# Kernel optimization log

Measured on AMD Instinct MI355X. Metric: run time of the kernel, lower is better.

The kernel has to match this reference:

```python
import jax, jax.numpy as jnp
import numpy as np

B, N, H, O = 2, 512, 128, 32  # batch, n_particles, hidden_dim, obs_dim


def _linear_init(key, out_d, in_d):
    kw, kb = jax.random.split(key)
    s = 1.0 / np.sqrt(in_d)
    W = jax.random.uniform(kw, (out_d, in_d), minval=-s, maxval=s, dtype=jnp.float32)
    b = jax.random.uniform(kb, (out_d,), minval=-s, maxval=s, dtype=jnp.float32)
    return W, b


def setup_inputs() -> dict:
    key = jax.random.key(0)
    ks = jax.random.split(key, 8)
    z = jax.random.normal(ks[0], (B, N, H), dtype=jnp.float32)
    s_t = jax.random.normal(ks[1], (B, N, O), dtype=jnp.float32)
    W1, b1 = _linear_init(ks[2], H, 2 * H)   # relation_mlp layer 0
    W2, b2 = _linear_init(ks[3], H, H)       # relation_mlp layer 2
    Wq, bq = _linear_init(ks[4], H, H)       # query_proj
    Wk, bk = _linear_init(ks[5], H, O)       # key_proj
    W3, b3 = _linear_init(ks[6], H, H)       # aggregation_mlp layer 0
    W4, b4 = _linear_init(ks[7], H, H)       # aggregation_mlp layer 2
    return dict(z=z, s_t=s_t, W1=W1, b1=b1, W2=W2, b2=b2, Wq=Wq, bq=bq,
                Wk=Wk, bk=bk, W3=W3, b3=b3, W4=W4, b4=b4)


def reference(z, s_t, W1, b1, W2, b2, Wq, bq, Wk, bk, W3, b3, W4, b4):
    b_, n, h = z.shape
    # query depends only on i, key only on j (repeat in the original is redundant)
    q = z @ Wq.T + bq            # [B,N,H]
    k = s_t @ Wk.T + bk          # [B,N,H]
    scores = jnp.einsum('bih,bjh->bij', q, k) / (h ** 0.5)   # [B,N,N]
    eye = jnp.eye(n, dtype=bool)
    scores = jnp.where(eye, -jnp.inf, scores)
    attn = jax.nn.softmax(scores, axis=-1)                   # [B,N,N]
    # relation_mlp on concat(z_i, z_j): split first weight into i- and j- halves
    W1i, W1j = W1[:, :h], W1[:, h:]
    zi = z @ W1i.T               # [B,N,H]
    zj = z @ W1j.T               # [B,N,H]
    rel = jnp.tanh(zi[:, :, None, :] + zj[:, None, :, :] + b1) @ W2.T + b2  # [B,N,N,H]
    agg = jnp.einsum('bij,bijh->bih', attn, rel)             # weighted sum over j
    dz_dt = jnp.tanh(agg @ W3.T + b3) @ W4.T + b4
    return dz_dt
```

## Files before the change

kernel.cpp:

```cpp
#include <hip/hip_runtime.h>
#include <hip/hip_bf16.h>

#define NN 512
#define HH 128
#define OO 32

#define KL 2.8853900817779268f

__device__ __forceinline__ float vexp2(float x) {
    float r; asm("v_exp_f32 %0, %1" : "=v"(r) : "v"(x)); return r;
}
__device__ __forceinline__ float vrcp(float x) {
    float r; asm("v_rcp_f32 %0, %1" : "=v"(r) : "v"(x)); return r;
}
__device__ __forceinline__ float tanh_fast(float x) {
    float e = vexp2(KL * x);
    return 1.0f - 2.0f * vrcp(e + 1.0f);
}
__device__ __forceinline__ float waveRedMax(float v) {
#pragma unroll
    for (int off = 32; off > 0; off >>= 1) v = fmaxf(v, __shfl_xor(v, off, 64));
    return v;
}
__device__ __forceinline__ float waveRedSum(float v) {
#pragma unroll
    for (int off = 32; off > 0; off >>= 1) v += __shfl_xor(v, off, 64);
    return v;
}
__device__ __forceinline__ float red8(float v) {
    v += __shfl_xor(v, 1, 64); v += __shfl_xor(v, 2, 64); v += __shfl_xor(v, 4, 64);
    return v;
}
__device__ __forceinline__ float dot16r(const float4* w, const float* x, int rot) {
    float a = 0;
#pragma unroll
    for (int ii = 0; ii < 4; ii++) {
        int i = (ii + rot) & 3;
        float4 xv = *(const float4*)(x + i * 4);
        a = fmaf(xv.x, w[ii].x, a); a = fmaf(xv.y, w[ii].y, a);
        a = fmaf(xv.z, w[ii].z, a); a = fmaf(xv.w, w[ii].w, a);
    }
    return a;
}
__device__ __forceinline__ unsigned short f2bf(float x) {
    unsigned u = __float_as_uint(x);
    u += 0x7fffu + ((u >> 16) & 1u);
    return (unsigned short)(u >> 16);
}
__device__ __forceinline__ float bf_lo(unsigned u) { return __uint_as_float((u & 0xffffu) << 16); }
__device__ __forceinline__ float bf_hi(unsigned u) { return __uint_as_float(u & 0xffff0000u); }

__global__ __launch_bounds__(1024, 4) void prep_kernel(
    const float* __restrict__ z, const float* __restrict__ s_t,
    const float* __restrict__ W1, const float* __restrict__ b1,
    const float* __restrict__ Wq, const float* __restrict__ bq,
    const float* __restrict__ Wk, const float* __restrict__ bk,
    float* __restrict__ qP, float* __restrict__ cP,
    unsigned short* __restrict__ EzjG, float* __restrict__ kTG) {
    __shared__ float zrow[4][HH];
    __shared__ float srow[4][OO];
    int t = threadIdx.x, bid = blockIdx.x;
    int r0 = bid * 4, b = bid >> 7, i0 = (bid & 127) * 4;
    int kq = t & 7, h = t >> 3, rot = (kq >> 1) & 3;

    const float4* WqP = (const float4*)(Wq + (size_t)h * HH) + kq * 4;
    const float4* WiP = (const float4*)(W1 + (size_t)h * 2 * HH) + kq * 4;
    const float4* WjP = (const float4*)(W1 + (size_t)h * 2 * HH + HH) + kq * 4;
    float4 wq[4], wi[4], wj[4];
#pragma unroll
    for (int ii = 0; ii < 4; ii++) {
        wq[ii] = WqP[(ii + rot) & 3];
        wi[ii] = WiP[(ii + rot) & 3];
        wj[ii] = WjP[(ii + rot) & 3];
    }
    float4 wk = ((const float4*)(Wk + (size_t)h * OO))[kq];
    float vbq = bq[h], vb1 = b1[h], vbk = bk[h];

    if (t < 4 * HH) zrow[t >> 7][t & 127] = z[(size_t)r0 * HH + t];
    else if (t < 4 * HH + 4 * OO) {
        int u = t - 4 * HH;
        srow[u >> 5][u & 31] = s_t[(size_t)r0 * OO + u];
    }
    __syncthreads();

    {
        float a0 = red8(dot16r(wq, &zrow[0][kq * 16], rot));
        float a1 = red8(dot16r(wq, &zrow[1][kq * 16], rot));
        float a2 = red8(dot16r(wq, &zrow[2][kq * 16], rot));
        float a3 = red8(dot16r(wq, &zrow[3][kq * 16], rot));
        if (kq == 0) {
            float* qp = qP + (size_t)bid * 512 + h * 4;
            qp[0] = a0 + vbq; qp[1] = a1 + vbq; qp[2] = a2 + vbq; qp[3] = a3 + vbq;
        }
    }
    {
        float a0 = red8(dot16r(wi, &zrow[0][kq * 16], rot));
        float a1 = red8(dot16r(wi, &zrow[1][kq * 16], rot));
        float a2 = red8(dot16r(wi, &zrow[2][kq * 16], rot));
        float a3 = red8(dot16r(wi, &zrow[3][kq * 16], rot));
        if (kq == 0) {
            float* cp = cP + (size_t)bid * 512 + h * 4;
            cp[0] = vexp2(KL * (a0 + vb1)); cp[1] = vexp2(KL * (a1 + vb1));
            cp[2] = vexp2(KL * (a2 + vb1)); cp[3] = vexp2(KL * (a3 + vb1));
        }
    }
    {
        float a0 = red8(dot16r(wj, &zrow[0][kq * 16], rot));
        float a1 = red8(dot16r(wj, &zrow[1][kq * 16], rot));
        float a2 = red8(dot16r(wj, &zrow[2][kq * 16], rot));
        float a3 = red8(dot16r(wj, &zrow[3][kq * 16], rot));
        if (kq == 0) {
            EzjG[(size_t)(r0 + 0) * HH + h] = f2bf(vexp2(KL * a0));
            EzjG[(size_t)(r0 + 1) * HH + h] = f2bf(vexp2(KL * a1));
            EzjG[(size_t)(r0 + 2) * HH + h] = f2bf(vexp2(KL * a2));
            EzjG[(size_t)(r0 + 3) * HH + h] = f2bf(vexp2(KL * a3));
        }
    }
    {
        float4 s0 = *(const float4*)&srow[0][kq * 4];
        float4 s1 = *(const float4*)&srow[1][kq * 4];
        float4 s2 = *(const float4*)&srow[2][kq * 4];
        float4 s3 = *(const float4*)&srow[3][kq * 4];
        float a0 = red8(s0.x * wk.x + s0.y * wk.y + s0.z * wk.z + s0.w * wk.w);
        float a1 = red8(s1.x * wk.x + s1.y * wk.y + s1.z * wk.z + s1.w * wk.w);
        float a2 = red8(s2.x * wk.x + s2.y * wk.y + s2.z * wk.z + s2.w * wk.w);
        float a3 = red8(s3.x * wk.x + s3.y * wk.y + s3.z * wk.z + s3.w * wk.w);
        if (kq == 0) {
            float4 kv = make_float4(a0 + vbk, a1 + vbk, a2 + vbk, a3 + vbk);
            *(float4*)(kTG + ((size_t)b * HH + h) * NN + i0) = kv;
        }
    }
}

__global__ __launch_bounds__(1024, 4) void fused_kernel(
    const float* __restrict__ qP, const float* __restrict__ cP,
    const float* __restrict__ kTG, const unsigned short* __restrict__ EzjG,
    const float* __restrict__ W2, const float* __restrict__ b2,
    const float* __restrict__ W3, const float* __restrict__ b3,
    const float* __restrict__ W4, const float* __restrict__ b4,
    float* __restrict__ out) {
    __shared__ float q4T[HH][4];
    __shared__ float c4T[HH][4];
    __shared__ float attnT[NN][4];
    __shared__ float buf[8192];
    __shared__ float UL[4][HH];
    __shared__ float aggL[4][HH];
    __shared__ float h1L[4][HH];
    __shared__ float redA[16], redB[16], redC[16], redD[16];

    float (*scp)[4][NN] = (float (*)[4][NN])buf;
    float (*part)[4][HH] = (float (*)[4][HH])buf;

    int t = threadIdx.x, bid = blockIdx.x;
    int b = bid >> 7, i0 = (bid & 127) * 4, r0 = bid * 4;

    if (t < 512) ((float*)q4T)[t] = qP[(size_t)bid * 512 + t];
    else         ((float*)c4T)[t - 512] = cP[(size_t)bid * 512 + (t - 512)];

    int j = t & 511, hs = t >> 9, h0 = hs * 64;
    const float* kb = kTG + ((size_t)b * HH + h0) * NN + j;
    float kv[32];
#pragma unroll
    for (int hh = 0; hh < 32; hh++) kv[hh] = kb[(size_t)hh * NN];
    __syncthreads();

    float s0 = 0, s1 = 0, s2 = 0, s3 = 0;
#pragma unroll
    for (int hh = 0; hh < 32; hh++) {
        float4 qv = *(const float4*)q4T[h0 + hh];
        s0 = fmaf(qv.x, kv[hh], s0); s1 = fmaf(qv.y, kv[hh], s1);
        s2 = fmaf(qv.z, kv[hh], s2); s3 = fmaf(qv.w, kv[hh], s3);
    }
#pragma unroll
    for (int hh = 0; hh < 32; hh++) kv[hh] = kb[(size_t)(32 + hh) * NN];
#pragma unroll
    for (int hh = 0; hh < 32; hh++) {
        float4 qv = *(const float4*)q4T[h0 + 32 + hh];
        s0 = fmaf(qv.x, kv[hh], s0); s1 = fmaf(qv.y, kv[hh], s1);
        s2 = fmaf(qv.z, kv[hh], s2); s3 = fmaf(qv.w, kv[hh], s3);
    }
    scp[hs][0][j] = s0; scp[hs][1][j] = s1;
    scp[hs][2][j] = s2; scp[hs][3][j] = s3;

    int lane6 = t & 63, qs = t >> 6, hp = lane6 * 2, jb = qs * 32;
    const unsigned* zbU = (const unsigned*)EzjG + (size_t)b * NN * (HH / 2) + lane6;
    unsigned uv[32];
#pragma unroll
    for (int jj = 0; jj < 32; jj++) uv[jj] = zbU[(size_t)(jb + jj) * (HH / 2)];
    __syncthreads();

    {
        int rp = t >> 9;
        int lr0 = rp * 2, lr1 = lr0 + 1;
        const float sc = 0.08838834764831845f;
        float c0 = (scp[0][lr0][j] + scp[1][lr0][j]) * sc;
        float c1 = (scp[0][lr1][j] + scp[1][lr1][j]) * sc;
        if (j == i0 + lr0) c0 = -1e30f;
        if (j == i0 + lr1) c1 = -1e30f;
        int lane = t & 63, w = t >> 6, wb = rp * 8;
        float m0 = waveRedMax(c0), m1 = waveRedMax(c1);
        if (lane == 0) { redA[w] = m0; redB[w] = m1; }
        __syncthreads();
        float mm0 = redA[wb], mm1 = redB[wb];
#pragma unroll
        for (int k = 1; k < 8; k++) { mm0 = fmaxf(mm0, redA[wb + k]); mm1 = fmaxf(mm1, redB[wb + k]); }
        float e0 = __expf(c0 - mm0), e1 = __expf(c1 - mm1);
        float p0 = waveRedSum(e0), p1 = waveRedSum(e1);
        if (lane == 0) { redC[w] = p0; redD[w] = p1; }
        __syncthreads();
        float S0 = redC[wb], S1 = redD[wb];
#pragma unroll
        for (int k = 1; k < 8; k++) { S0 += redC[wb + k]; S1 += redD[wb + k]; }
        attnT[j][lr0] = e0 * __fdividef(1.0f, S0);
        attnT[j][lr1] = e1 * __fdividef(1.0f, S1);
    }
    __syncthreads();

    {
        float4 cA = *(const float4*)c4T[hp];
        float4 cB = *(const float4*)c4T[hp + 1];
        float a0A = 0, a1A = 0, a2A = 0, a3A = 0;
        float a0B = 0, a1B = 0, a2B = 0, a3B = 0;
#pragma unroll
        for (int jj = 0; jj < 32; jj++) {
            int jc = jb + jj;
            float Ex = bf_lo(uv[jj]), Ey = bf_hi(uv[jj]);
            float4 w = *(const float4*)attnT[jc];
            a0A = fmaf(w.x, vrcp(fmaf(cA.x, Ex, 1.0f)), a0A);
            a1A = fmaf(w.y, vrcp(fmaf(cA.y, Ex, 1.0f)), a1A);
            a2A = fmaf(w.z, vrcp(fmaf(cA.z, Ex, 1.0f)), a2A);
            a3A = fmaf(w.w, vrcp(fmaf(cA.w, Ex, 1.0f)), a3A);
            a0B = fmaf(w.x, vrcp(fmaf(cB.x, Ey, 1.0f)), a0B);
            a1B = fmaf(w.y, vrcp(fmaf(cB.y, Ey, 1.0f)), a1B);
            a2B = fmaf(w.z, vrcp(fmaf(cB.z, Ey, 1.0f)), a2B);
            a3B = fmaf(w.w, vrcp(fmaf(cB.w, Ey, 1.0f)), a3B);
        }
        *(float2*)&part[qs][0][hp] = make_float2(a0A, a0B);
        *(float2*)&part[qs][1][hp] = make_float2(a1A, a1B);
        *(float2*)&part[qs][2][hp] = make_float2(a2A, a2B);
        *(float2*)&part[qs][3][hp] = make_float2(a3A, a3B);
    }

    int kq = t & 7, h8 = t >> 3, rot = (kq >> 1) & 3;
    const float4* W2p = (const float4*)(W2 + (size_t)h8 * HH) + kq * 4;
    const float4* W3p = (const float4*)(W3 + (size_t)h8 * HH) + kq * 4;
    const float4* W4p = (const float4*)(W4 + (size_t)h8 * HH) + kq * 4;
    float4 w2[4], w3[4], w4[4];
#pragma unroll
    for (int ii = 0; ii < 4; ii++) {
        w2[ii] = W2p[(ii + rot) & 3];
        w3[ii] = W3p[(ii + rot) & 3];
        w4[ii] = W4p[(ii + rot) & 3];
    }
    float vb2 = b2[h8], vb3 = b3[h8], vb4 = b4[h8];
    __syncthreads();

    if (t < 512) {
        int r = t >> 7, h = t & 127;
        float s = 0;
#pragma unroll
        for (int q = 0; q < 16; q++) s += part[q][r][h];
        UL[r][h] = fmaf(-2.0f, s, 1.0f);
    }
    __syncthreads();

    {
        float a0 = red8(dot16r(w2, &UL[0][kq * 16], rot));
        float a1 = red8(dot16r(w2, &UL[1][kq * 16], rot));
        float a2 = red8(dot16r(w2, &UL[2][kq * 16], rot));
        float a3 = red8(dot16r(w2, &UL[3][kq * 16], rot));
        if (kq == 0) {
            aggL[0][h8] = a0 + vb2; aggL[1][h8] = a1 + vb2;
            aggL[2][h8] = a2 + vb2; aggL[3][h8] = a3 + vb2;
        }
    }
    __syncthreads();
    {
        float a0 = red8(dot16r(w3, &aggL[0][kq * 16], rot));
        float a1 = red8(dot16r(w3, &aggL[1][kq * 16], rot));
        float a2 = red8(dot16r(w3, &aggL[2][kq * 16], rot));
        float a3 = red8(dot16r(w3, &aggL[3][kq * 16], rot));
        if (kq == 0) {
            h1L[0][h8] = tanh_fast(a0 + vb3); h1L[1][h8] = tanh_fast(a1 + vb3);
            h1L[2][h8] = tanh_fast(a2 + vb3); h1L[3][h8] = tanh_fast(a3 + vb3);
        }
    }
    __syncthreads();
    {
        float a0 = red8(dot16r(w4, &h1L[0][kq * 16], rot));
        float a1 = red8(dot16r(w4, &h1L[1][kq * 16], rot));
        float a2 = red8(dot16r(w4, &h1L[2][kq * 16], rot));
        float a3 = red8(dot16r(w4, &h1L[3][kq * 16], rot));
        if (kq == 0) {
            out[(size_t)(r0 + 0) * HH + h8] = a0 + vb4;
            out[(size_t)(r0 + 1) * HH + h8] = a1 + vb4;
            out[(size_t)(r0 + 2) * HH + h8] = a2 + vb4;
            out[(size_t)(r0 + 3) * HH + h8] = a3 + vb4;
        }
    }
}

extern "C" void kernel_launch(void* const* d_in, const int* in_sizes, int n_in,
                              void* d_out, int out_size, void* d_ws, size_t ws_size,
                              hipStream_t stream) {
    const float* z   = (const float*)d_in[0];
    const float* s_t = (const float*)d_in[1];
    const float* W1  = (const float*)d_in[2];
    const float* b1  = (const float*)d_in[3];
    const float* W2  = (const float*)d_in[4];
    const float* b2  = (const float*)d_in[5];
    const float* Wq  = (const float*)d_in[6];
    const float* bq  = (const float*)d_in[7];
    const float* Wk  = (const float*)d_in[8];
    const float* bk  = (const float*)d_in[9];
    const float* W3  = (const float*)d_in[10];
    const float* b3  = (const float*)d_in[11];
    const float* W4  = (const float*)d_in[12];
    const float* b4  = (const float*)d_in[13];
    float* out = (float*)d_out;

    float* ws = (float*)d_ws;
    float* kT = ws;
    float* qP = ws + 131072;
    float* cP = ws + 262144;
    unsigned short* Ezj = (unsigned short*)(ws + 393216);

    hipLaunchKernelGGL(prep_kernel, dim3(256), dim3(1024), 0, stream,
                       z, s_t, W1, b1, Wq, bq, Wk, bk, qP, cP, Ezj, kT);
    hipLaunchKernelGGL(fused_kernel, dim3(256), dim3(1024), 0, stream,
                       qP, cP, kT, Ezj, W2, b2, W3, b3, W4, b4, out);
}
```

Measured before the change: 35.51 us.

## Split fused kernel to two query rows per block and double grid size

The fused kernel now processes 2 query rows per block instead of 4, launching 512 blocks instead of 256. The prep kernel writes q and c in the matching 2-row packed layout. Register-staged preloads of keys and Ezj are replaced with streaming loads inside partially unrolled loops, and launch bounds are raised to allow more resident blocks. The aim is to fill more compute units and raise occupancy. The cost is that every block re-reads the full kT and Ezj tiles and the MLP weights, so global and L2 traffic roughly doubles and the preloads no longer hide load latency.

```diff
diff --git a/kernel.cpp b/kernel.cpp
--- a/kernel.cpp
+++ b/kernel.cpp
@@ -89,8 +89,9 @@
         float a2 = red8(dot16r(wq, &zrow[2][kq * 16], rot));
         float a3 = red8(dot16r(wq, &zrow[3][kq * 16], rot));
         if (kq == 0) {
-            float* qp = qP + (size_t)bid * 512 + h * 4;
-            qp[0] = a0 + vbq; qp[1] = a1 + vbq; qp[2] = a2 + vbq; qp[3] = a3 + vbq;
+            float* qp = qP + (size_t)(r0 >> 1) * 256 + h * 2;
+            qp[0] = a0 + vbq; qp[1] = a1 + vbq;
+            qp[256] = a2 + vbq; qp[257] = a3 + vbq;
         }
     }
     {
@@ -99,9 +100,9 @@
         float a2 = red8(dot16r(wi, &zrow[2][kq * 16], rot));
         float a3 = red8(dot16r(wi, &zrow[3][kq * 16], rot));
         if (kq == 0) {
-            float* cp = cP + (size_t)bid * 512 + h * 4;
+            float* cp = cP + (size_t)(r0 >> 1) * 256 + h * 2;
             cp[0] = vexp2(KL * (a0 + vb1)); cp[1] = vexp2(KL * (a1 + vb1));
-            cp[2] = vexp2(KL * (a2 + vb1)); cp[3] = vexp2(KL * (a3 + vb1));
+            cp[256] = vexp2(KL * (a2 + vb1)); cp[257] = vexp2(KL * (a3 + vb1));
         }
     }
     {
@@ -132,130 +133,92 @@
     }
 }
 
-__global__ __launch_bounds__(1024, 4) void fused_kernel(
+__global__ __launch_bounds__(1024, 8) void fused_kernel(
     const float* __restrict__ qP, const float* __restrict__ cP,
     const float* __restrict__ kTG, const unsigned short* __restrict__ EzjG,
     const float* __restrict__ W2, const float* __restrict__ b2,
     const float* __restrict__ W3, const float* __restrict__ b3,
     const float* __restrict__ W4, const float* __restrict__ b4,
     float* __restrict__ out) {
-    __shared__ float q4T[HH][4];
-    __shared__ float c4T[HH][4];
-    __shared__ float attnT[NN][4];
-    __shared__ float buf[8192];
-    __shared__ float UL[4][HH];
-    __shared__ float aggL[4][HH];
-    __shared__ float h1L[4][HH];
-    __shared__ float redA[16], redB[16], redC[16], redD[16];
-
-    float (*scp)[4][NN] = (float (*)[4][NN])buf;
-    float (*part)[4][HH] = (float (*)[4][HH])buf;
+    __shared__ float q2T[HH][2];
+    __shared__ float c2T[HH][2];
+    __shared__ float attnT[NN][2];
+    __shared__ float buf[4096];
+    __shared__ float UL[2][HH];
+    __shared__ float aggL[2][HH];
+    __shared__ float h1L[2][HH];
+    __shared__ float redA[16], redB[16];
+
+    float (*scp)[2][NN] = (float (*)[2][NN])buf;
+    float (*part)[2][HH] = (float (*)[2][HH])buf;
 
     int t = threadIdx.x, bid = blockIdx.x;
-    int b = bid >> 7, i0 = (bid & 127) * 4, r0 = bid * 4;
-
-    if (t < 512) ((float*)q4T)[t] = qP[(size_t)bid * 512 + t];
-    else         ((float*)c4T)[t - 512] = cP[(size_t)bid * 512 + (t - 512)];
-
-    int j = t & 511, hs = t >> 9, h0 = hs * 64;
-    const float* kb = kTG + ((size_t)b * HH + h0) * NN + j;
-    float kv[32];
-#pragma unroll
-    for (int hh = 0; hh < 32; hh++) kv[hh] = kb[(size_t)hh * NN];
-    __syncthreads();
-
-    float s0 = 0, s1 = 0, s2 = 0, s3 = 0;
-#pragma unroll
-    for (int hh = 0; hh < 32; hh++) {
-        float4 qv = *(const float4*)q4T[h0 + hh];
-        s0 = fmaf(qv.x, kv[hh], s0); s1 = fmaf(qv.y, kv[hh], s1);
-        s2 = fmaf(qv.z, kv[hh], s2); s3 = fmaf(qv.w, kv[hh], s3);
-    }
-#pragma unroll
-    for (int hh = 0; hh < 32; hh++) kv[hh] = kb[(size_t)(32 + hh) * NN];
-#pragma unroll
-    for (int hh = 0; hh < 32; hh++) {
-        float4 qv = *(const float4*)q4T[h0 + 32 + hh];
-        s0 = fmaf(qv.x, kv[hh], s0); s1 = fmaf(qv.y, kv[hh], s1);
-        s2 = fmaf(qv.z, kv[hh], s2); s3 = fmaf(qv.w, kv[hh], s3);
-    }
-    scp[hs][0][j] = s0; scp[hs][1][j] = s1;
-    scp[hs][2][j] = s2; scp[hs][3][j] = s3;
-
-    int lane6 = t & 63, qs = t >> 6, hp = lane6 * 2, jb = qs * 32;
-    const unsigned* zbU = (const unsigned*)EzjG + (size_t)b * NN * (HH / 2) + lane6;
-    unsigned uv[32];
-#pragma unroll
-    for (int jj = 0; jj < 32; jj++) uv[jj] = zbU[(size_t)(jb + jj) * (HH / 2)];
-    __syncthreads();
-
-    {
-        int rp = t >> 9;
-        int lr0 = rp * 2, lr1 = lr0 + 1;
+    int b = bid >> 8, i0 = (bid & 255) * 2, r0 = bid * 2;
+
+    if (t < 256)      ((float*)q2T)[t] = qP[(size_t)bid * 256 + t];
+    else if (t < 512) ((float*)c2T)[t - 256] = cP[(size_t)bid * 256 + (t - 256)];
+    __syncthreads();
+
+    int j = t & 511;
+    {
+        int hs = t >> 9, h0 = hs * 64;
+        const float* kb = kTG + ((size_t)b * HH + h0) * NN + j;
+        float s0 = 0, s1 = 0;
+#pragma unroll 8
+        for (int hh = 0; hh < 64; hh++) {
+            float kv = kb[(size_t)hh * NN];
+            float2 qv = *(const float2*)q2T[h0 + hh];
+            s0 = fmaf(qv.x, kv, s0); s1 = fmaf(qv.y, kv, s1);
+        }
+        scp[hs][0][j] = s0; scp[hs][1][j] = s1;
+    }
+    __syncthreads();
+
+    {
+        int r = t >> 9;
         const float sc = 0.08838834764831845f;
-        float c0 = (scp[0][lr0][j] + scp[1][lr0][j]) * sc;
-        float c1 = (scp[0][lr1][j] + scp[1][lr1][j]) * sc;
-        if (j == i0 + lr0) c0 = -1e30f;
-        if (j == i0 + lr1) c1 = -1e30f;
-        int lane = t & 63, w = t >> 6, wb = rp * 8;
-        float m0 = waveRedMax(c0), m1 = waveRedMax(c1);
-        if (lane == 0) { redA[w] = m0; redB[w] = m1; }
+        float s = (scp[0][r][j] + scp[1][r][j]) * sc;
+        if (j == i0 + r) s = -1e30f;
+        int lane = t & 63, w = t >> 6, wb = r * 8;
+        float m = waveRedMax(s);
+        if (lane == 0) redA[w] = m;
         __syncthreads();
-        float mm0 = redA[wb], mm1 = redB[wb];
-#pragma unroll
-        for (int k = 1; k < 8; k++) { mm0 = fmaxf(mm0, redA[wb + k]); mm1 = fmaxf(mm1, redB[wb + k]); }
-        float e0 = __expf(c0 - mm0), e1 = __expf(c1 - mm1);
-        float p0 = waveRedSum(e0), p1 = waveRedSum(e1);
-        if (lane == 0) { redC[w] = p0; redD[w] = p1; }
+        float mm = redA[wb];
+#pragma unroll
+        for (int k = 1; k < 8; k++) mm = fmaxf(mm, redA[wb + k]);
+        float e = __expf(s - mm);
+        float p = waveRedSum(e);
+        if (lane == 0) redB[w] = p;
         __syncthreads();
-        float S0 = redC[wb], S1 = redD[wb];
-#pragma unroll
-        for (int k = 1; k < 8; k++) { S0 += redC[wb + k]; S1 += redD[wb + k]; }
-        attnT[j][lr0] = e0 * __fdividef(1.0f, S0);
-        attnT[j][lr1] = e1 * __fdividef(1.0f, S1);
-    }
-    __syncthreads();
-
-    {
-        float4 cA = *(const float4*)c4T[hp];
-        float4 cB = *(const float4*)c4T[hp + 1];
-        float a0A = 0, a1A = 0, a2A = 0, a3A = 0;
-        float a0B = 0, a1B = 0, a2B = 0, a3B = 0;
-#pragma unroll
+        float S = redB[wb];
+#pragma unroll
+        for (int k = 1; k < 8; k++) S += redB[wb + k];
+        attnT[j][r] = e * __fdividef(1.0f, S);
+    }
+    __syncthreads();
+
+    {
+        int lane6 = t & 63, qs = t >> 6, hp = lane6 * 2, jb = qs * 32;
+        const unsigned* zbU = (const unsigned*)EzjG + (size_t)b * NN * 64 + lane6;
+        float2 cA = *(const float2*)c2T[hp];
+        float2 cB = *(const float2*)c2T[hp + 1];
+        float a0A = 0, a1A = 0, a0B = 0, a1B = 0;
+#pragma unroll 8
         for (int jj = 0; jj < 32; jj++) {
             int jc = jb + jj;
-            float Ex = bf_lo(uv[jj]), Ey = bf_hi(uv[jj]);
-            float4 w = *(const float4*)attnT[jc];
+            unsigned u = zbU[(size_t)jc * 64];
+            float Ex = bf_lo(u), Ey = bf_hi(u);
+            float2 w = *(const float2*)attnT[jc];
             a0A = fmaf(w.x, vrcp(fmaf(cA.x, Ex, 1.0f)), a0A);
             a1A = fmaf(w.y, vrcp(fmaf(cA.y, Ex, 1.0f)), a1A);
-            a2A = fmaf(w.z, vrcp(fmaf(cA.z, Ex, 1.0f)), a2A);
-            a3A = fmaf(w.w, vrcp(fmaf(cA.w, Ex, 1.0f)), a3A);
             a0B = fmaf(w.x, vrcp(fmaf(cB.x, Ey, 1.0f)), a0B);
             a1B = fmaf(w.y, vrcp(fmaf(cB.y, Ey, 1.0f)), a1B);
-            a2B = fmaf(w.z, vrcp(fmaf(cB.z, Ey, 1.0f)), a2B);
-            a3B = fmaf(w.w, vrcp(fmaf(cB.w, Ey, 1.0f)), a3B);
         }
         *(float2*)&part[qs][0][hp] = make_float2(a0A, a0B);
         *(float2*)&part[qs][1][hp] = make_float2(a1A, a1B);
-        *(float2*)&part[qs][2][hp] = make_float2(a2A, a2B);
-        *(float2*)&part[qs][3][hp] = make_float2(a3A, a3B);
-    }
-
-    int kq = t & 7, h8 = t >> 3, rot = (kq >> 1) & 3;
-    const float4* W2p = (const float4*)(W2 + (size_t)h8 * HH) + kq * 4;
-    const float4* W3p = (const float4*)(W3 + (size_t)h8 * HH) + kq * 4;
-    const float4* W4p = (const float4*)(W4 + (size_t)h8 * HH) + kq * 4;
-    float4 w2[4], w3[4], w4[4];
-#pragma unroll
-    for (int ii = 0; ii < 4; ii++) {
-        w2[ii] = W2p[(ii + rot) & 3];
-        w3[ii] = W3p[(ii + rot) & 3];
-        w4[ii] = W4p[(ii + rot) & 3];
-    }
-    float vb2 = b2[h8], vb3 = b3[h8], vb4 = b4[h8];
-    __syncthreads();
-
-    if (t < 512) {
+    }
+    __syncthreads();
+    if (t < 256) {
         int r = t >> 7, h = t & 127;
         float s = 0;
 #pragma unroll
@@ -265,37 +228,43 @@
     __syncthreads();
 
     {
-        float a0 = red8(dot16r(w2, &UL[0][kq * 16], rot));
-        float a1 = red8(dot16r(w2, &UL[1][kq * 16], rot));
-        float a2 = red8(dot16r(w2, &UL[2][kq * 16], rot));
-        float a3 = red8(dot16r(w2, &UL[3][kq * 16], rot));
-        if (kq == 0) {
-            aggL[0][h8] = a0 + vb2; aggL[1][h8] = a1 + vb2;
-            aggL[2][h8] = a2 + vb2; aggL[3][h8] = a3 + vb2;
-        }
-    }
-    __syncthreads();
-    {
-        float a0 = red8(dot16r(w3, &aggL[0][kq * 16], rot));
-        float a1 = red8(dot16r(w3, &aggL[1][kq * 16], rot));
-        float a2 = red8(dot16r(w3, &aggL[2][kq * 16], rot));
-        float a3 = red8(dot16r(w3, &aggL[3][kq * 16], rot));
-        if (kq == 0) {
-            h1L[0][h8] = tanh_fast(a0 + vb3); h1L[1][h8] = tanh_fast(a1 + vb3);
-            h1L[2][h8] = tanh_fast(a2 + vb3); h1L[3][h8] = tanh_fast(a3 + vb3);
-        }
-    }
-    __syncthreads();
-    {
-        float a0 = red8(dot16r(w4, &h1L[0][kq * 16], rot));
-        float a1 = red8(dot16r(w4, &h1L[1][kq * 16], rot));
-        float a2 = red8(dot16r(w4, &h1L[2][kq * 16], rot));
-        float a3 = red8(dot16r(w4, &h1L[3][kq * 16], rot));
-        if (kq == 0) {
-            out[(size_t)(r0 + 0) * HH + h8] = a0 + vb4;
-            out[(size_t)(r0 + 1) * HH + h8] = a1 + vb4;
-            out[(size_t)(r0 + 2) * HH + h8] = a2 + vb4;
-            out[(size_t)(r0 + 3) * HH + h8] = a3 + vb4;
+        int kq = t & 7, h8 = t >> 3, rot = (kq >> 1) & 3;
+        float4 w[4];
+        {
+            const float4* Wp = (const float4*)(W2 + (size_t)h8 * HH) + kq * 4;
+#pragma unroll
+            for (int ii = 0; ii < 4; ii++) w[ii] = Wp[(ii + rot) & 3];
+            float a0 = red8(dot16r(w, &UL[0][kq * 16], rot));
+            float a1 = red8(dot16r(w, &UL[1][kq * 16], rot));
+            if (kq == 0) {
+                float vb = b2[h8];
+                aggL[0][h8] = a0 + vb; aggL[1][h8] = a1 + vb;
+            }
+        }
+        __syncthreads();
+        {
+            const float4* Wp = (const float4*)(W3 + (size_t)h8 * HH) + kq * 4;
+#pragma unroll
+            for (int ii = 0; ii < 4; ii++) w[ii] = Wp[(ii + rot) & 3];
+            float a0 = red8(dot16r(w, &aggL[0][kq * 16], rot));
+            float a1 = red8(dot16r(w, &aggL[1][kq * 16], rot));
+            if (kq == 0) {
+                float vb = b3[h8];
+                h1L[0][h8] = tanh_fast(a0 + vb); h1L[1][h8] = tanh_fast(a1 + vb);
+            }
+        }
+        __syncthreads();
+        {
+            const float4* Wp = (const float4*)(W4 + (size_t)h8 * HH) + kq * 4;
+#pragma unroll
+            for (int ii = 0; ii < 4; ii++) w[ii] = Wp[(ii + rot) & 3];
+            float a0 = red8(dot16r(w, &h1L[0][kq * 16], rot));
+            float a1 = red8(dot16r(w, &h1L[1][kq * 16], rot));
+            if (kq == 0) {
+                float vb = b4[h8];
+                out[(size_t)(r0 + 0) * HH + h8] = a0 + vb;
+                out[(size_t)(r0 + 1) * HH + h8] = a1 + vb;
+            }
         }
     }
 }
@@ -327,6 +296,6 @@
 
     hipLaunchKernelGGL(prep_kernel, dim3(256), dim3(1024), 0, stream,
                        z, s_t, W1, b1, Wq, bq, Wk, bk, qP, cP, Ezj, kT);
-    hipLaunchKernelGGL(fused_kernel, dim3(256), dim3(1024), 0, stream,
+    hipLaunchKernelGGL(fused_kernel, dim3(512), dim3(1024), 0, stream,
                        qP, cP, kT, Ezj, W2, b2, W3, b3, W4, b4, out);
 }
```

Result: slower. 42.67 us (+20.2%).
